# Kernel optimization log

Hardware: AMD Instinct MI355X
Metric: run time of the kernel (lower is better)

## Reference

```python
import jax, jax.numpy as jnp
import numpy as np

B, D, H = 16384, 32, 128

def setup_inputs() -> dict:
    key = jax.random.key(0)
    ks = jax.random.split(key, 6)
    x_t = jax.random.normal(ks[0], (B, D), jnp.float32)
    t = jax.random.uniform(ks[1], (B, 1), jnp.float32)
    beta = jax.random.uniform(ks[2], (B, 1), jnp.float32)
    W1 = jax.random.normal(ks[3], (D + 1, H), jnp.float32) * (1.0 / np.sqrt(D + 1))
    b1 = jnp.zeros((H,), jnp.float32)
    W2 = jax.random.normal(ks[4], (H, D), jnp.float32) * (1.0 / np.sqrt(H))
    b2 = jnp.zeros((D,), jnp.float32)
    return {"x_t": x_t, "t": t, "beta": beta, "W1": W1, "b1": b1, "W2": W2, "b2": b2}

def reference(x_t, t, beta, W1, b1, W2, b2):
    # Score network s = f(x_t, t): in the torch module s is a tensor carrying
    # an autograd graph through x_t and t; here we make that function explicit.
    def s_of(x, tt):
        h = jnp.tanh(jnp.concatenate([x, tt], axis=-1) @ W1 + b1)
        return h @ W2 + b2  # [B, D]

    d = x_t.shape[-1]

    def div_x(x, tt):
        # exact divergence: trace of Jacobian d s / d x, via D forward-mode passes
        eye = jnp.eye(d, dtype=x.dtype)
        def one_dir(e):  # e: [D] basis vector
            _, jv = jax.jvp(lambda xx: s_of(xx, tt), (x,), (jnp.broadcast_to(e, x.shape),))
            return jnp.sum(jv * e, axis=-1)  # picks J[:, i, i] -> [B]
        return jnp.sum(jax.vmap(one_dir)(eye), axis=0)[:, None]  # [B, 1]

    s = s_of(x_t, t)

    # ds/dt per batch element (t is [B,1], batch elements independent)
    _, ds_dt = jax.jvp(lambda tt: s_of(x_t, tt), (t,), (jnp.ones_like(t),))  # [B, D]

    # grad_x of per-batch scalar: div_x(s) + |s|^2 + x . s
    def scalar_sum(xx):
        ss = s_of(xx, t)
        val = div_x(xx, t) + jnp.sum(ss * ss, axis=1, keepdims=True) \
              + jnp.sum(xx * ss, axis=1, keepdims=True)  # [B, 1]
        return jnp.sum(val)
    grad_x = jax.grad(scalar_sum)(x_t)  # [B, D]

    resid = ds_dt - 0.5 * beta * grad_x
    # metric == 'L1'
    loss = jnp.mean(jnp.abs(resid), axis=1)[:, None]  # [B, 1]
    return loss
```

## Files before the change

kernel.cpp:

```cpp
#include <hip/hip_runtime.h>
#include <math.h>

namespace {

typedef _Float16 f16;
typedef _Float16 f16x8 __attribute__((ext_vector_type(8)));
typedef _Float16 f16x4 __attribute__((ext_vector_type(4)));
typedef float    f32x4 __attribute__((ext_vector_type(4)));

constexpr int D  = 32;
constexpr int H  = 128;
constexpr int S1 = 40;
constexpr int S2 = 136;
constexpr int THREADS = 256;
constexpr int BPW = 16;
constexpr int BPB = 64;

__device__ __forceinline__ float fast_tanh(float z) {
  float e = __expf(2.0f * z);
  return 1.0f - 2.0f * __builtin_amdgcn_rcpf(e + 1.0f);
}

__device__ __forceinline__ f32x4 mfma16(f16x8 a, f16x8 b, f32x4 c) {
  return __builtin_amdgcn_mfma_f32_16x16x32_f16(a, b, c, 0, 0, 0);
}

__global__ __launch_bounds__(THREADS, 1) void fpe_mfma(
    const float* __restrict__ xg, const float* __restrict__ tg,
    const float* __restrict__ betag, const float* __restrict__ W1g,
    const float* __restrict__ b1g, const float* __restrict__ W2g,
    const float* __restrict__ b2g, float* __restrict__ out, int Btot)
{
  __shared__ alignas(16) f16 W1T[H * S1];
  __shared__ alignas(16) f16 W1X[D * S2];
  __shared__ alignas(16) f16 W2R[H * S1];
  __shared__ alignas(16) f16 W2T[D * S2];
  __shared__ alignas(16) float b1s[H];
  __shared__ alignas(16) float cks[H];
  __shared__ alignas(16) float b2s[D];
  __shared__ alignas(16) f16  w132h[H];
  __shared__ alignas(16) f16 pbuf[4][BPW * S2];
  __shared__ alignas(16) f16 vbuf[4][BPW * S1];

  const int tid = threadIdx.x;

  for (int n = tid; n < D * H; n += THREADS) {
    int i = n >> 7, k = n & (H - 1);
    f16 w = (f16)W1g[n];
    W1T[k * S1 + i] = w;
    W1X[i * S2 + k] = w;
  }
  for (int n = tid; n < H * D; n += THREADS) {
    int k = n >> 5, j = n & (D - 1);
    f16 w = (f16)W2g[n];
    W2R[k * S1 + j] = w;
    W2T[j * S2 + k] = w;
  }
  if (tid < H) { w132h[tid] = (f16)W1g[D * H + tid]; b1s[tid] = b1g[tid]; }
  if (tid < D) b2s[tid] = b2g[tid];
  __syncthreads();
  if (tid < H) {
    float c = 0.f;
    #pragma unroll
    for (int j = 0; j < D; ++j)
      c += (float)W1T[tid * S1 + j] * (float)W2R[tid * S1 + j];
    cks[tid] = c;
  }
  __syncthreads();

  const int wv  = tid >> 6;
  const int ln  = tid & 63;
  const int col = ln & 15;
  const int g4  = ln >> 4;
  const int b0  = blockIdx.x * BPB + wv * BPW;
  if (b0 >= Btot) return;
  const int batch = min(b0 + col, Btot - 1);

  f16* pb = pbuf[wv];
  f16* vb = vbuf[wv];

  const float* xrow = xg + (size_t)batch * D;
  const float4 xk0 = *(const float4*)(xrow + 8 * g4);
  const float4 xk1 = *(const float4*)(xrow + 8 * g4 + 4);
  const float4 xc0 = *(const float4*)(xrow + 4 * g4);
  const float4 xc1 = *(const float4*)(xrow + 16 + 4 * g4);
  const float tval = tg[batch];
  const float hb   = 0.5f * betag[batch];

  f16x8 bx;
  bx[0] = (f16)xk0.x; bx[1] = (f16)xk0.y; bx[2] = (f16)xk0.z; bx[3] = (f16)xk0.w;
  bx[4] = (f16)xk1.x; bx[5] = (f16)xk1.y; bx[6] = (f16)xk1.z; bx[7] = (f16)xk1.w;

  float hC[8][4];
  #pragma unroll
  for (int hm = 0; hm < 8; ++hm) {
    f16x8 a = *(const f16x8*)&W1T[(16 * hm + col) * S1 + 8 * g4];
    f32x4 zero = {0.f, 0.f, 0.f, 0.f};
    f32x4 z = mfma16(a, bx, zero);
    float4 b1v = *(const float4*)&b1s[16 * hm + 4 * g4];
    f16x4 wtv  = *(const f16x4*)&w132h[16 * hm + 4 * g4];
    f16x4 hv;
    #pragma unroll
    for (int r = 0; r < 4; ++r) {
      float zz = z[r] + ((const float*)&b1v)[r] + (float)wtv[r] * tval;
      float hh = fast_tanh(zz);
      hC[hm][r] = hh;
      hv[r] = (f16)hh;
    }
    *(f16x4*)&pb[col * S2 + 16 * hm + 4 * g4] = hv;
  }

  f32x4 sT[2], dT[2];
  sT[0] = {0.f,0.f,0.f,0.f}; sT[1] = {0.f,0.f,0.f,0.f};
  dT[0] = {0.f,0.f,0.f,0.f}; dT[1] = {0.f,0.f,0.f,0.f};
  #pragma unroll
  for (int ks = 0; ks < 4; ++ks) {
    f16x8 hvf = *(const f16x8*)&pb[col * S2 + 32 * ks + 8 * g4];
    f16x8 wv8 = *(const f16x8*)&w132h[32 * ks + 8 * g4];
    f16x8 rv;
    #pragma unroll
    for (int r = 0; r < 8; ++r) {
      float hf = (float)hvf[r];
      float gg = fmaf(-hf, hf, 1.0f);
      rv[r] = (f16)(gg * (float)wv8[r]);
    }
    #pragma unroll
    for (int om = 0; om < 2; ++om) {
      f16x8 a = *(const f16x8*)&W2T[(16 * om + col) * S2 + 32 * ks + 8 * g4];
      sT[om] = mfma16(a, hvf, sT[om]);
      dT[om] = mfma16(a, rv,  dT[om]);
    }
  }
  #pragma unroll
  for (int om = 0; om < 2; ++om) {
    float4 b2v = *(const float4*)&b2s[16 * om + 4 * g4];
    float4 xcv = om ? xc1 : xc0;
    f16x4 vv;
    #pragma unroll
    for (int r = 0; r < 4; ++r) {
      sT[om][r] += ((const float*)&b2v)[r];
      vv[r] = (f16)fmaf(2.0f, sT[om][r], ((const float*)&xcv)[r]);
    }
    *(f16x4*)&vb[col * S1 + 16 * om + 4 * g4] = vv;
  }

  {
    f16x8 bv = *(const f16x8*)&vb[col * S1 + 8 * g4];
    #pragma unroll
    for (int hm = 0; hm < 8; ++hm) {
      f16x8 a = *(const f16x8*)&W2R[(16 * hm + col) * S1 + 8 * g4];
      f32x4 zero = {0.f, 0.f, 0.f, 0.f};
      f32x4 m = mfma16(a, bv, zero);
      float4 cv = *(const float4*)&cks[16 * hm + 4 * g4];
      f16x4 qv;
      #pragma unroll
      for (int r = 0; r < 4; ++r) {
        float hh = hC[hm][r];
        float gg = fmaf(-hh, hh, 1.0f);
        float mm = fmaf(-2.0f * ((const float*)&cv)[r], hh, m[r]);
        qv[r] = (f16)(gg * mm);
      }
      *(f16x4*)&pb[col * S2 + 16 * hm + 4 * g4] = qv;
    }
  }

  f32x4 gT[2];
  gT[0] = {0.f,0.f,0.f,0.f}; gT[1] = {0.f,0.f,0.f,0.f};
  #pragma unroll
  for (int ks = 0; ks < 4; ++ks) {
    f16x8 q8 = *(const f16x8*)&pb[col * S2 + 32 * ks + 8 * g4];
    #pragma unroll
    for (int om = 0; om < 2; ++om) {
      f16x8 a = *(const f16x8*)&W1X[(16 * om + col) * S2 + 32 * ks + 8 * g4];
      gT[om] = mfma16(a, q8, gT[om]);
    }
  }

  float acc = 0.f;
  #pragma unroll
  for (int om = 0; om < 2; ++om)
    #pragma unroll
    for (int r = 0; r < 4; ++r)
      acc += fabsf(dT[om][r] - hb * (sT[om][r] + gT[om][r]));
  acc += __shfl_xor(acc, 16);
  acc += __shfl_xor(acc, 32);
  if (ln < BPW && (b0 + ln) < Btot) out[b0 + ln] = acc * (1.0f / 32.0f);
}

}

extern "C" void kernel_launch(void* const* d_in, const int* in_sizes, int n_in,
                              void* d_out, int out_size, void* d_ws, size_t ws_size,
                              hipStream_t stream) {
  const float* x    = (const float*)d_in[0];
  const float* t    = (const float*)d_in[1];
  const float* beta = (const float*)d_in[2];
  const float* W1   = (const float*)d_in[3];
  const float* b1   = (const float*)d_in[4];
  const float* W2   = (const float*)d_in[5];
  const float* b2   = (const float*)d_in[6];
  float* out = (float*)d_out;

  const int Btot = in_sizes[1];
  const int grid = (Btot + BPB - 1) / BPB;
  hipLaunchKernelGGL(fpe_mfma, dim3(grid), dim3(THREADS), 0, stream,
                     x, t, beta, W1, b1, W2, b2, out, Btot);
}
```

Before: 10.41 us.

## Split each 16-row batch tile across two waves and vectorize weight staging

Each 16-sample tile is now processed by a pair of waves, each handling half of the hidden and output dimensions. The halves exchange intermediates through shared memory with block barriers and combine partial L1 sums at the end. Block batch size halves, so the grid doubles and per-wave serial MFMA/tanh work halves. Weight loading now uses float4 global reads, the ck dot product reads vectors, and the r vector is precomputed in the first stage. The cost is more block barriers, and the per-block weight staging is repeated across twice as many blocks.

```diff
diff --git a/kernel.cpp b/kernel.cpp
--- a/kernel.cpp
+++ b/kernel.cpp
@@ -11,10 +11,10 @@
 constexpr int D  = 32;
 constexpr int H  = 128;
 constexpr int S1 = 40;
-constexpr int S2 = 136;
+constexpr int S2 = 152;
 constexpr int THREADS = 256;
-constexpr int BPW = 16;
-constexpr int BPB = 64;
+constexpr int BPP = 16;
+constexpr int BPB = 32;
 
 __device__ __forceinline__ float fast_tanh(float z) {
   float e = __expf(2.0f * z);
@@ -25,129 +25,137 @@
   return __builtin_amdgcn_mfma_f32_16x16x32_f16(a, b, c, 0, 0, 0);
 }
 
-__global__ __launch_bounds__(THREADS, 1) void fpe_mfma(
+__global__ __launch_bounds__(THREADS, 1) void fpe_mfma2(
     const float* __restrict__ xg, const float* __restrict__ tg,
     const float* __restrict__ betag, const float* __restrict__ W1g,
     const float* __restrict__ b1g, const float* __restrict__ W2g,
     const float* __restrict__ b2g, float* __restrict__ out, int Btot)
 {
   __shared__ alignas(16) f16 W1T[H * S1];
+  __shared__ alignas(16) f16 W2R[H * S1];
   __shared__ alignas(16) f16 W1X[D * S2];
-  __shared__ alignas(16) f16 W2R[H * S1];
   __shared__ alignas(16) f16 W2T[D * S2];
   __shared__ alignas(16) float b1s[H];
   __shared__ alignas(16) float cks[H];
   __shared__ alignas(16) float b2s[D];
   __shared__ alignas(16) f16  w132h[H];
-  __shared__ alignas(16) f16 pbuf[4][BPW * S2];
-  __shared__ alignas(16) f16 vbuf[4][BPW * S1];
+  __shared__ alignas(16) f16 hbuf[2][BPP * S2];
+  __shared__ alignas(16) f16 rbuf[2][BPP * S2];
+  __shared__ alignas(16) f16 vbuf[2][BPP * S1];
+  __shared__ float accb[2][2][16];
 
   const int tid = threadIdx.x;
 
-  for (int n = tid; n < D * H; n += THREADS) {
-    int i = n >> 7, k = n & (H - 1);
-    f16 w = (f16)W1g[n];
-    W1T[k * S1 + i] = w;
-    W1X[i * S2 + k] = w;
-  }
-  for (int n = tid; n < H * D; n += THREADS) {
-    int k = n >> 5, j = n & (D - 1);
-    f16 w = (f16)W2g[n];
-    W2R[k * S1 + j] = w;
-    W2T[j * S2 + k] = w;
+  for (int n4 = tid; n4 < (D * H) / 4; n4 += THREADS) {
+    float4 w = ((const float4*)W1g)[n4];
+    int flat = n4 * 4, i = flat >> 7, k = flat & 127;
+    f16x4 w4 = {(f16)w.x, (f16)w.y, (f16)w.z, (f16)w.w};
+    W1T[(k + 0) * S1 + i] = w4[0];
+    W1T[(k + 1) * S1 + i] = w4[1];
+    W1T[(k + 2) * S1 + i] = w4[2];
+    W1T[(k + 3) * S1 + i] = w4[3];
+    *(f16x4*)&W1X[i * S2 + k] = w4;
+  }
+  for (int n4 = tid; n4 < (H * D) / 4; n4 += THREADS) {
+    float4 w = ((const float4*)W2g)[n4];
+    int flat = n4 * 4, k = flat >> 5, j = flat & 31;
+    f16x4 w4 = {(f16)w.x, (f16)w.y, (f16)w.z, (f16)w.w};
+    *(f16x4*)&W2R[k * S1 + j] = w4;
+    W2T[(j + 0) * S2 + k] = w4[0];
+    W2T[(j + 1) * S2 + k] = w4[1];
+    W2T[(j + 2) * S2 + k] = w4[2];
+    W2T[(j + 3) * S2 + k] = w4[3];
   }
   if (tid < H) { w132h[tid] = (f16)W1g[D * H + tid]; b1s[tid] = b1g[tid]; }
   if (tid < D) b2s[tid] = b2g[tid];
   __syncthreads();
+
   if (tid < H) {
     float c = 0.f;
     #pragma unroll
-    for (int j = 0; j < D; ++j)
-      c += (float)W1T[tid * S1 + j] * (float)W2R[tid * S1 + j];
+    for (int q = 0; q < 4; ++q) {
+      f16x8 a = *(const f16x8*)&W1T[tid * S1 + 8 * q];
+      f16x8 b = *(const f16x8*)&W2R[tid * S1 + 8 * q];
+      #pragma unroll
+      for (int r = 0; r < 8; ++r) c += (float)a[r] * (float)b[r];
+    }
     cks[tid] = c;
   }
   __syncthreads();
 
-  const int wv  = tid >> 6;
-  const int ln  = tid & 63;
-  const int col = ln & 15;
-  const int g4  = ln >> 4;
-  const int b0  = blockIdx.x * BPB + wv * BPW;
-  if (b0 >= Btot) return;
+  const int wv   = tid >> 6;
+  const int ln   = tid & 63;
+  const int pi   = wv >> 1;
+  const int half = wv & 1;
+  const int col  = ln & 15;
+  const int g4   = ln >> 4;
+  const int b0   = blockIdx.x * BPB + pi * BPP;
   const int batch = min(b0 + col, Btot - 1);
 
-  f16* pb = pbuf[wv];
-  f16* vb = vbuf[wv];
+  f16* hb = hbuf[pi];
+  f16* rb = rbuf[pi];
+  f16* vb = vbuf[pi];
 
   const float* xrow = xg + (size_t)batch * D;
   const float4 xk0 = *(const float4*)(xrow + 8 * g4);
   const float4 xk1 = *(const float4*)(xrow + 8 * g4 + 4);
-  const float4 xc0 = *(const float4*)(xrow + 4 * g4);
-  const float4 xc1 = *(const float4*)(xrow + 16 + 4 * g4);
+  const float4 xcv = *(const float4*)(xrow + 16 * half + 4 * g4);
   const float tval = tg[batch];
-  const float hb   = 0.5f * betag[batch];
+  const float hbeta = 0.5f * betag[batch];
 
   f16x8 bx;
   bx[0] = (f16)xk0.x; bx[1] = (f16)xk0.y; bx[2] = (f16)xk0.z; bx[3] = (f16)xk0.w;
   bx[4] = (f16)xk1.x; bx[5] = (f16)xk1.y; bx[6] = (f16)xk1.z; bx[7] = (f16)xk1.w;
 
-  float hC[8][4];
-  #pragma unroll
-  for (int hm = 0; hm < 8; ++hm) {
+  float hC[4][4];
+  #pragma unroll
+  for (int n = 0; n < 4; ++n) {
+    const int hm = 4 * half + n;
     f16x8 a = *(const f16x8*)&W1T[(16 * hm + col) * S1 + 8 * g4];
     f32x4 zero = {0.f, 0.f, 0.f, 0.f};
     f32x4 z = mfma16(a, bx, zero);
     float4 b1v = *(const float4*)&b1s[16 * hm + 4 * g4];
     f16x4 wtv  = *(const f16x4*)&w132h[16 * hm + 4 * g4];
-    f16x4 hv;
+    f16x4 hv, rv;
     #pragma unroll
     for (int r = 0; r < 4; ++r) {
       float zz = z[r] + ((const float*)&b1v)[r] + (float)wtv[r] * tval;
       float hh = fast_tanh(zz);
-      hC[hm][r] = hh;
+      hC[n][r] = hh;
       hv[r] = (f16)hh;
-    }
-    *(f16x4*)&pb[col * S2 + 16 * hm + 4 * g4] = hv;
-  }
-
-  f32x4 sT[2], dT[2];
-  sT[0] = {0.f,0.f,0.f,0.f}; sT[1] = {0.f,0.f,0.f,0.f};
-  dT[0] = {0.f,0.f,0.f,0.f}; dT[1] = {0.f,0.f,0.f,0.f};
+      rv[r] = (f16)(fmaf(-hh, hh, 1.0f) * (float)wtv[r]);
+    }
+    *(f16x4*)&hb[col * S2 + 16 * hm + 4 * g4] = hv;
+    *(f16x4*)&rb[col * S2 + 16 * hm + 4 * g4] = rv;
+  }
+  __syncthreads();
+
+  f32x4 sT = {0.f, 0.f, 0.f, 0.f}, dT = {0.f, 0.f, 0.f, 0.f};
   #pragma unroll
   for (int ks = 0; ks < 4; ++ks) {
-    f16x8 hvf = *(const f16x8*)&pb[col * S2 + 32 * ks + 8 * g4];
-    f16x8 wv8 = *(const f16x8*)&w132h[32 * ks + 8 * g4];
-    f16x8 rv;
-    #pragma unroll
-    for (int r = 0; r < 8; ++r) {
-      float hf = (float)hvf[r];
-      float gg = fmaf(-hf, hf, 1.0f);
-      rv[r] = (f16)(gg * (float)wv8[r]);
-    }
-    #pragma unroll
-    for (int om = 0; om < 2; ++om) {
-      f16x8 a = *(const f16x8*)&W2T[(16 * om + col) * S2 + 32 * ks + 8 * g4];
-      sT[om] = mfma16(a, hvf, sT[om]);
-      dT[om] = mfma16(a, rv,  dT[om]);
-    }
-  }
-  #pragma unroll
-  for (int om = 0; om < 2; ++om) {
-    float4 b2v = *(const float4*)&b2s[16 * om + 4 * g4];
-    float4 xcv = om ? xc1 : xc0;
+    f16x8 hvf = *(const f16x8*)&hb[col * S2 + 32 * ks + 8 * g4];
+    f16x8 rvf = *(const f16x8*)&rb[col * S2 + 32 * ks + 8 * g4];
+    f16x8 a   = *(const f16x8*)&W2T[(16 * half + col) * S2 + 32 * ks + 8 * g4];
+    sT = mfma16(a, hvf, sT);
+    dT = mfma16(a, rvf, dT);
+  }
+  {
+    float4 b2v = *(const float4*)&b2s[16 * half + 4 * g4];
     f16x4 vv;
     #pragma unroll
     for (int r = 0; r < 4; ++r) {
-      sT[om][r] += ((const float*)&b2v)[r];
-      vv[r] = (f16)fmaf(2.0f, sT[om][r], ((const float*)&xcv)[r]);
-    }
-    *(f16x4*)&vb[col * S1 + 16 * om + 4 * g4] = vv;
-  }
+      sT[r] += ((const float*)&b2v)[r];
+      vv[r] = (f16)fmaf(2.0f, sT[r], ((const float*)&xcv)[r]);
+    }
+    *(f16x4*)&vb[col * S1 + 16 * half + 4 * g4] = vv;
+  }
+  __syncthreads();
 
   {
     f16x8 bv = *(const f16x8*)&vb[col * S1 + 8 * g4];
     #pragma unroll
-    for (int hm = 0; hm < 8; ++hm) {
+    for (int n = 0; n < 4; ++n) {
+      const int hm = 4 * half + n;
       f16x8 a = *(const f16x8*)&W2R[(16 * hm + col) * S1 + 8 * g4];
       f32x4 zero = {0.f, 0.f, 0.f, 0.f};
       f32x4 m = mfma16(a, bv, zero);
@@ -155,36 +163,36 @@
       f16x4 qv;
       #pragma unroll
       for (int r = 0; r < 4; ++r) {
-        float hh = hC[hm][r];
-        float gg = fmaf(-hh, hh, 1.0f);
+        float hh = hC[n][r];
         float mm = fmaf(-2.0f * ((const float*)&cv)[r], hh, m[r]);
-        qv[r] = (f16)(gg * mm);
+        qv[r] = (f16)(fmaf(-hh, hh, 1.0f) * mm);
       }
-      *(f16x4*)&pb[col * S2 + 16 * hm + 4 * g4] = qv;
-    }
-  }
-
-  f32x4 gT[2];
-  gT[0] = {0.f,0.f,0.f,0.f}; gT[1] = {0.f,0.f,0.f,0.f};
+      *(f16x4*)&hb[col * S2 + 16 * hm + 4 * g4] = qv;
+    }
+  }
+  __syncthreads();
+
+  f32x4 gT = {0.f, 0.f, 0.f, 0.f};
   #pragma unroll
   for (int ks = 0; ks < 4; ++ks) {
-    f16x8 q8 = *(const f16x8*)&pb[col * S2 + 32 * ks + 8 * g4];
-    #pragma unroll
-    for (int om = 0; om < 2; ++om) {
-      f16x8 a = *(const f16x8*)&W1X[(16 * om + col) * S2 + 32 * ks + 8 * g4];
-      gT[om] = mfma16(a, q8, gT[om]);
-    }
+    f16x8 q8 = *(const f16x8*)&hb[col * S2 + 32 * ks + 8 * g4];
+    f16x8 a  = *(const f16x8*)&W1X[(16 * half + col) * S2 + 32 * ks + 8 * g4];
+    gT = mfma16(a, q8, gT);
   }
 
   float acc = 0.f;
   #pragma unroll
-  for (int om = 0; om < 2; ++om)
-    #pragma unroll
-    for (int r = 0; r < 4; ++r)
-      acc += fabsf(dT[om][r] - hb * (sT[om][r] + gT[om][r]));
+  for (int r = 0; r < 4; ++r)
+    acc += fabsf(dT[r] - hbeta * (sT[r] + gT[r]));
   acc += __shfl_xor(acc, 16);
   acc += __shfl_xor(acc, 32);
-  if (ln < BPW && (b0 + ln) < Btot) out[b0 + ln] = acc * (1.0f / 32.0f);
+  if (ln < 16) accb[pi][half][ln] = acc;
+  __syncthreads();
+  if (half == 0 && ln < 16) {
+    int b = b0 + ln;
+    if (b < Btot)
+      out[b] = (accb[pi][0][ln] + accb[pi][1][ln]) * (1.0f / 32.0f);
+  }
 }
 
 }
@@ -203,6 +211,6 @@
 
   const int Btot = in_sizes[1];
   const int grid = (Btot + BPB - 1) / BPB;
-  hipLaunchKernelGGL(fpe_mfma, dim3(grid), dim3(THREADS), 0, stream,
+  hipLaunchKernelGGL(fpe_mfma2, dim3(grid), dim3(THREADS), 0, stream,
                      x, t, beta, W1, b1, W2, b2, out, Btot);
 }
```

After: 11.71 us. +12.5%, slower.

## Read weight MFMA fragments directly from global memory instead of staging in LDS

Applied to the files above, without the earlier changes.

Removes the per-block prologue that converts and transposes W1/W2 into shared memory, with its two barriers. Each wave now loads weight fragments straight from global (cache-resident) memory and converts them to fp16 just before every MFMA. The tanh-derivative-times-w_t vector is precomputed in the first layer and kept in a separate LDS buffer. The trade is many small strided global loads, some non-coalesced, in place of LDS reads, plus partial loop unrolling.

```diff
diff --git a/kernel.cpp b/kernel.cpp
--- a/kernel.cpp
+++ b/kernel.cpp
@@ -10,10 +10,9 @@
 
 constexpr int D  = 32;
 constexpr int H  = 128;
+constexpr int S2 = 152;
 constexpr int S1 = 40;
-constexpr int S2 = 136;
 constexpr int THREADS = 256;
-constexpr int BPW = 16;
 constexpr int BPB = 64;
 
 __device__ __forceinline__ float fast_tanh(float z) {
@@ -25,116 +24,96 @@
   return __builtin_amdgcn_mfma_f32_16x16x32_f16(a, b, c, 0, 0, 0);
 }
 
-__global__ __launch_bounds__(THREADS, 1) void fpe_mfma(
+__global__ __launch_bounds__(THREADS, 1) void fpe_g(
     const float* __restrict__ xg, const float* __restrict__ tg,
     const float* __restrict__ betag, const float* __restrict__ W1g,
     const float* __restrict__ b1g, const float* __restrict__ W2g,
     const float* __restrict__ b2g, float* __restrict__ out, int Btot)
 {
-  __shared__ alignas(16) f16 W1T[H * S1];
-  __shared__ alignas(16) f16 W1X[D * S2];
-  __shared__ alignas(16) f16 W2R[H * S1];
-  __shared__ alignas(16) f16 W2T[D * S2];
-  __shared__ alignas(16) float b1s[H];
+  __shared__ alignas(16) f16 hbuf[4][16 * S2];
+  __shared__ alignas(16) f16 rbuf[4][16 * S2];
+  __shared__ alignas(16) f16 vbuf[4][16 * S1];
   __shared__ alignas(16) float cks[H];
-  __shared__ alignas(16) float b2s[D];
-  __shared__ alignas(16) f16  w132h[H];
-  __shared__ alignas(16) f16 pbuf[4][BPW * S2];
-  __shared__ alignas(16) f16 vbuf[4][BPW * S1];
 
   const int tid = threadIdx.x;
-
-  for (int n = tid; n < D * H; n += THREADS) {
-    int i = n >> 7, k = n & (H - 1);
-    f16 w = (f16)W1g[n];
-    W1T[k * S1 + i] = w;
-    W1X[i * S2 + k] = w;
-  }
-  for (int n = tid; n < H * D; n += THREADS) {
-    int k = n >> 5, j = n & (D - 1);
-    f16 w = (f16)W2g[n];
-    W2R[k * S1 + j] = w;
-    W2T[j * S2 + k] = w;
-  }
-  if (tid < H) { w132h[tid] = (f16)W1g[D * H + tid]; b1s[tid] = b1g[tid]; }
-  if (tid < D) b2s[tid] = b2g[tid];
-  __syncthreads();
-  if (tid < H) {
-    float c = 0.f;
-    #pragma unroll
-    for (int j = 0; j < D; ++j)
-      c += (float)W1T[tid * S1 + j] * (float)W2R[tid * S1 + j];
-    cks[tid] = c;
-  }
-  __syncthreads();
-
   const int wv  = tid >> 6;
   const int ln  = tid & 63;
   const int col = ln & 15;
   const int g4  = ln >> 4;
-  const int b0  = blockIdx.x * BPB + wv * BPW;
-  if (b0 >= Btot) return;
+  const int b0  = blockIdx.x * BPB + wv * 16;
   const int batch = min(b0 + col, Btot - 1);
-
-  f16* pb = pbuf[wv];
-  f16* vb = vbuf[wv];
 
   const float* xrow = xg + (size_t)batch * D;
   const float4 xk0 = *(const float4*)(xrow + 8 * g4);
   const float4 xk1 = *(const float4*)(xrow + 8 * g4 + 4);
   const float4 xc0 = *(const float4*)(xrow + 4 * g4);
   const float4 xc1 = *(const float4*)(xrow + 16 + 4 * g4);
-  const float tval = tg[batch];
-  const float hb   = 0.5f * betag[batch];
+  const float tval  = tg[batch];
+  const float hbeta = 0.5f * betag[batch];
 
   f16x8 bx;
   bx[0] = (f16)xk0.x; bx[1] = (f16)xk0.y; bx[2] = (f16)xk0.z; bx[3] = (f16)xk0.w;
   bx[4] = (f16)xk1.x; bx[5] = (f16)xk1.y; bx[6] = (f16)xk1.z; bx[7] = (f16)xk1.w;
 
+  if (tid < H) {
+    const float* w2row = W2g + tid * D;
+    float c0 = 0.f, c1 = 0.f;
+    #pragma unroll
+    for (int j = 0; j < D; j += 2) {
+      c0 = fmaf(W1g[j * H + tid],       w2row[j],     c0);
+      c1 = fmaf(W1g[(j + 1) * H + tid], w2row[j + 1], c1);
+    }
+    cks[tid] = c0 + c1;
+  }
+  __syncthreads();
+
+  f16* hb = hbuf[wv];
+  f16* rb = rbuf[wv];
+  f16* vb = vbuf[wv];
+
   float hC[8][4];
-  #pragma unroll
+  #pragma unroll 2
   for (int hm = 0; hm < 8; ++hm) {
-    f16x8 a = *(const f16x8*)&W1T[(16 * hm + col) * S1 + 8 * g4];
-    f32x4 zero = {0.f, 0.f, 0.f, 0.f};
-    f32x4 z = mfma16(a, bx, zero);
-    float4 b1v = *(const float4*)&b1s[16 * hm + 4 * g4];
-    f16x4 wtv  = *(const f16x4*)&w132h[16 * hm + 4 * g4];
-    f16x4 hv;
+    const float* ap = W1g + (8 * g4) * H + 16 * hm + col;
+    f16x8 af;
+    #pragma unroll
+    for (int j = 0; j < 8; ++j) af[j] = (f16)ap[j * H];
+    f32x4 z = mfma16(af, bx, f32x4{0.f, 0.f, 0.f, 0.f});
+    const float4 b1v = *(const float4*)(b1g + 16 * hm + 4 * g4);
+    const float4 wtv = *(const float4*)(W1g + D * H + 16 * hm + 4 * g4);
+    f16x4 hv, rv;
     #pragma unroll
     for (int r = 0; r < 4; ++r) {
-      float zz = z[r] + ((const float*)&b1v)[r] + (float)wtv[r] * tval;
+      float zz = z[r] + ((const float*)&b1v)[r] + ((const float*)&wtv)[r] * tval;
       float hh = fast_tanh(zz);
       hC[hm][r] = hh;
       hv[r] = (f16)hh;
+      rv[r] = (f16)(fmaf(-hh, hh, 1.0f) * ((const float*)&wtv)[r]);
     }
-    *(f16x4*)&pb[col * S2 + 16 * hm + 4 * g4] = hv;
+    *(f16x4*)&hb[col * S2 + 16 * hm + 4 * g4] = hv;
+    *(f16x4*)&rb[col * S2 + 16 * hm + 4 * g4] = rv;
   }
 
-  f32x4 sT[2], dT[2];
-  sT[0] = {0.f,0.f,0.f,0.f}; sT[1] = {0.f,0.f,0.f,0.f};
-  dT[0] = {0.f,0.f,0.f,0.f}; dT[1] = {0.f,0.f,0.f,0.f};
-  #pragma unroll
+  f32x4 sT[2] = {{0.f,0.f,0.f,0.f}, {0.f,0.f,0.f,0.f}};
+  f32x4 dT[2] = {{0.f,0.f,0.f,0.f}, {0.f,0.f,0.f,0.f}};
+  #pragma unroll 2
   for (int ks = 0; ks < 4; ++ks) {
-    f16x8 hvf = *(const f16x8*)&pb[col * S2 + 32 * ks + 8 * g4];
-    f16x8 wv8 = *(const f16x8*)&w132h[32 * ks + 8 * g4];
-    f16x8 rv;
-    #pragma unroll
-    for (int r = 0; r < 8; ++r) {
-      float hf = (float)hvf[r];
-      float gg = fmaf(-hf, hf, 1.0f);
-      rv[r] = (f16)(gg * (float)wv8[r]);
-    }
+    f16x8 hvf = *(const f16x8*)&hb[col * S2 + 32 * ks + 8 * g4];
+    f16x8 rvf = *(const f16x8*)&rb[col * S2 + 32 * ks + 8 * g4];
     #pragma unroll
     for (int om = 0; om < 2; ++om) {
-      f16x8 a = *(const f16x8*)&W2T[(16 * om + col) * S2 + 32 * ks + 8 * g4];
-      sT[om] = mfma16(a, hvf, sT[om]);
-      dT[om] = mfma16(a, rv,  dT[om]);
+      const float* ap = W2g + (32 * ks + 8 * g4) * D + 16 * om + col;
+      f16x8 af;
+      #pragma unroll
+      for (int jj = 0; jj < 8; ++jj) af[jj] = (f16)ap[jj * D];
+      sT[om] = mfma16(af, hvf, sT[om]);
+      dT[om] = mfma16(af, rvf, dT[om]);
     }
   }
   #pragma unroll
   for (int om = 0; om < 2; ++om) {
-    float4 b2v = *(const float4*)&b2s[16 * om + 4 * g4];
-    float4 xcv = om ? xc1 : xc0;
+    const float4 b2v = *(const float4*)(b2g + 16 * om + 4 * g4);
+    const float4 xcv = om ? xc1 : xc0;
     f16x4 vv;
     #pragma unroll
     for (int r = 0; r < 4; ++r) {
@@ -146,33 +125,40 @@
 
   {
     f16x8 bv = *(const f16x8*)&vb[col * S1 + 8 * g4];
-    #pragma unroll
+    #pragma unroll 2
     for (int hm = 0; hm < 8; ++hm) {
-      f16x8 a = *(const f16x8*)&W2R[(16 * hm + col) * S1 + 8 * g4];
-      f32x4 zero = {0.f, 0.f, 0.f, 0.f};
-      f32x4 m = mfma16(a, bv, zero);
-      float4 cv = *(const float4*)&cks[16 * hm + 4 * g4];
+      const float* ap = W2g + (16 * hm + col) * D + 8 * g4;
+      const float4 a0 = *(const float4*)ap;
+      const float4 a1 = *(const float4*)(ap + 4);
+      f16x8 af;
+      af[0]=(f16)a0.x; af[1]=(f16)a0.y; af[2]=(f16)a0.z; af[3]=(f16)a0.w;
+      af[4]=(f16)a1.x; af[5]=(f16)a1.y; af[6]=(f16)a1.z; af[7]=(f16)a1.w;
+      f32x4 m = mfma16(af, bv, f32x4{0.f, 0.f, 0.f, 0.f});
+      const float4 cv = *(const float4*)&cks[16 * hm + 4 * g4];
       f16x4 qv;
       #pragma unroll
       for (int r = 0; r < 4; ++r) {
         float hh = hC[hm][r];
-        float gg = fmaf(-hh, hh, 1.0f);
         float mm = fmaf(-2.0f * ((const float*)&cv)[r], hh, m[r]);
-        qv[r] = (f16)(gg * mm);
+        qv[r] = (f16)(fmaf(-hh, hh, 1.0f) * mm);
       }
-      *(f16x4*)&pb[col * S2 + 16 * hm + 4 * g4] = qv;
+      *(f16x4*)&hb[col * S2 + 16 * hm + 4 * g4] = qv;
     }
   }
 
-  f32x4 gT[2];
-  gT[0] = {0.f,0.f,0.f,0.f}; gT[1] = {0.f,0.f,0.f,0.f};
-  #pragma unroll
+  f32x4 gT[2] = {{0.f,0.f,0.f,0.f}, {0.f,0.f,0.f,0.f}};
+  #pragma unroll 2
   for (int ks = 0; ks < 4; ++ks) {
-    f16x8 q8 = *(const f16x8*)&pb[col * S2 + 32 * ks + 8 * g4];
+    f16x8 q8 = *(const f16x8*)&hb[col * S2 + 32 * ks + 8 * g4];
     #pragma unroll
     for (int om = 0; om < 2; ++om) {
-      f16x8 a = *(const f16x8*)&W1X[(16 * om + col) * S2 + 32 * ks + 8 * g4];
-      gT[om] = mfma16(a, q8, gT[om]);
+      const float* ap = W1g + (16 * om + col) * H + 32 * ks + 8 * g4;
+      const float4 a0 = *(const float4*)ap;
+      const float4 a1 = *(const float4*)(ap + 4);
+      f16x8 af;
+      af[0]=(f16)a0.x; af[1]=(f16)a0.y; af[2]=(f16)a0.z; af[3]=(f16)a0.w;
+      af[4]=(f16)a1.x; af[5]=(f16)a1.y; af[6]=(f16)a1.z; af[7]=(f16)a1.w;
+      gT[om] = mfma16(af, q8, gT[om]);
     }
   }
 
@@ -181,10 +167,10 @@
   for (int om = 0; om < 2; ++om)
     #pragma unroll
     for (int r = 0; r < 4; ++r)
-      acc += fabsf(dT[om][r] - hb * (sT[om][r] + gT[om][r]));
+      acc += fabsf(dT[om][r] - hbeta * (sT[om][r] + gT[om][r]));
   acc += __shfl_xor(acc, 16);
   acc += __shfl_xor(acc, 32);
-  if (ln < BPW && (b0 + ln) < Btot) out[b0 + ln] = acc * (1.0f / 32.0f);
+  if (ln < 16 && (b0 + ln) < Btot) out[b0 + ln] = acc * (1.0f / 32.0f);
 }
 
 }
@@ -203,6 +189,6 @@
 
   const int Btot = in_sizes[1];
   const int grid = (Btot + BPB - 1) / BPB;
-  hipLaunchKernelGGL(fpe_mfma, dim3(grid), dim3(THREADS), 0, stream,
+  hipLaunchKernelGGL(fpe_g, dim3(grid), dim3(THREADS), 0, stream,
                      x, t, beta, W1, b1, W2, b2, out, Btot);
 }
```

Measured after the change: 14.11 us. +35.5%, slower.
